# Kernel tuning notes

Hardware: AMD Instinct MI355X
Metric: run time of the kernel (lower is better)

Reference implementation:

```python
import jax, jax.numpy as jnp
import numpy as np

B, L, D, K = 8, 256, 256, 64  # batch, slots, n_input, attn_dimension


def setup_inputs() -> dict:
    key = jax.random.key(0)
    k1, k2, k3 = jax.random.split(key, 3)
    inputs = jax.random.normal(k1, (B, L, D), dtype=jnp.float32)
    # torch.nn.Linear weights are [out_features, in_features]; scale to avoid tanh saturation
    W1 = jax.random.normal(k2, (K, 2 * D), dtype=jnp.float32) * (1.0 / np.sqrt(2 * D))
    W2 = jax.random.normal(k3, (1, K), dtype=jnp.float32) * (1.0 / np.sqrt(K))
    return {"inputs": inputs, "W1": W1, "W2": W2}


def reference(inputs, W1, W2):
    # CONCAT branch of SlotAttention:
    #   score[b,i,j] = W2 @ tanh(W1 @ concat(inputs[b,i], inputs[b,j]))
    # Split W1 into the halves acting on the i-part and j-part of the concat
    # (identical math, avoids materializing the [B,L,L,2D] concat tensor).
    d = inputs.shape[-1]
    W1i, W1j = W1[:, :d], W1[:, d:]
    qi = jnp.einsum('bld,kd->blk', inputs, W1i)          # [B,L,K]
    kj = jnp.einsum('bld,kd->blk', inputs, W1j)          # [B,L,K]
    h = jnp.tanh(qi[:, :, None, :] + kj[:, None, :, :])  # [B,L,L,K]
    scores = jnp.einsum('bijk,k->bij', h, W2[0])         # [B,L,L]
    attn = jax.nn.softmax(scores, axis=2)                # softmax over j
    context = jnp.einsum('bij,bjd->bid', attn, inputs)   # [B,L,D]
    return jnp.concatenate([inputs, context], axis=2)    # [B,L,2D]
```

## Files before the change

### kernel.cpp

```cpp
#include <hip/hip_runtime.h>


#define Bn 8
#define Ln 256
#define Dn 256
#define Kn 64
#define ROWS (Bn*Ln)
#define IPB 4

__global__ __launch_bounds__(128) void proj_kernel(
    const float* __restrict__ X,
    const float* __restrict__ W1,
    float* __restrict__ QK)
{
    __shared__ float Xs[4 * 256];
    const int tid = threadIdx.x;
    const int r0 = blockIdx.x * 4;

    const float4* Xg4 = (const float4*)(X + r0 * Dn);
    float4* Xs4 = (float4*)Xs;
    #pragma unroll
    for (int idx = tid; idx < 256; idx += 128) Xs4[idx] = Xg4[idx];
    __syncthreads();

    const int k = tid & 63, half = tid >> 6;
    const float4* Wrow = (const float4*)(W1 + k * (2 * Dn) + half * Dn);
    float acc[4] = {0, 0, 0, 0};
    #pragma unroll 8
    for (int d4 = 0; d4 < 64; ++d4) {
        float4 w = Wrow[d4];
        #pragma unroll
        for (int r = 0; r < 4; ++r) {
            float4 x = ((const float4*)(Xs + r * Dn))[d4];
            float a = acc[r];
            a = fmaf(w.x, x.x, a);
            a = fmaf(w.y, x.y, a);
            a = fmaf(w.z, x.z, a);
            a = fmaf(w.w, x.w, a);
            acc[r] = a;
        }
    }
    #pragma unroll
    for (int r = 0; r < 4; ++r) {
        float e = __expf(2.0f * acc[r]);
        float t = 1.0f - 2.0f / (e + 1.0f);
        t = fminf(0.99999988f, fmaxf(-0.99999988f, t));
        QK[(r0 + r) * 128 + tid] = t;
    }
}

__global__ __launch_bounds__(256) void attn_kernel(
    const float* __restrict__ X,
    const float* __restrict__ QK,
    const float* __restrict__ W2,
    float* __restrict__ out)
{
    __shared__ float tq_s[IPB * Kn];
    __shared__ float w2_s[Kn];
    __shared__ float S[Ln * IPB];
    __shared__ float4 red[4 * IPB * 64];

    const int tid = threadIdx.x;
    const int b  = blockIdx.x / (Ln / IPB);
    const int i0 = (blockIdx.x % (Ln / IPB)) * IPB;

    if (tid < Kn) w2_s[tid] = W2[tid];
    {
        int ii = tid >> 6, kk = tid & 63;
        tq_s[ii * Kn + kk] = QK[(b * Ln + i0 + ii) * 128 + kk];
    }

    float tkr[Kn];
    const float4* kj4 = (const float4*)(QK + (b * Ln + tid) * 128 + 64);
    #pragma unroll
    for (int q = 0; q < 16; ++q) {
        float4 v = kj4[q];
        tkr[q * 4 + 0] = v.x; tkr[q * 4 + 1] = v.y;
        tkr[q * 4 + 2] = v.z; tkr[q * 4 + 3] = v.w;
    }
    __syncthreads();

    float s[IPB] = {0, 0, 0, 0};
    const float4* w4  = (const float4*)w2_s;
    const float4* q4a = (const float4*)(tq_s);
    const float4* q4b = (const float4*)(tq_s + Kn);
    const float4* q4c = (const float4*)(tq_s + 2 * Kn);
    const float4* q4d = (const float4*)(tq_s + 3 * Kn);
    #pragma unroll
    for (int k4 = 0; k4 < 16; ++k4) {
        float4 w  = w4[k4];
        float4 q0 = q4a[k4], q1 = q4b[k4], q2 = q4c[k4], q3 = q4d[k4];
        #pragma unroll
        for (int c = 0; c < 4; ++c) {
            float tk = tkr[k4 * 4 + c];
            float wk = (c == 0) ? w.x : (c == 1) ? w.y : (c == 2) ? w.z : w.w;
            float tq0 = (c == 0) ? q0.x : (c == 1) ? q0.y : (c == 2) ? q0.z : q0.w;
            float tq1 = (c == 0) ? q1.x : (c == 1) ? q1.y : (c == 2) ? q1.z : q1.w;
            float tq2 = (c == 0) ? q2.x : (c == 1) ? q2.y : (c == 2) ? q2.z : q2.w;
            float tq3 = (c == 0) ? q3.x : (c == 1) ? q3.y : (c == 2) ? q3.z : q3.w;
            float n0 = tq0 + tk, d0 = fmaf(tq0, tk, 1.0f);
            float n1 = tq1 + tk, d1 = fmaf(tq1, tk, 1.0f);
            float n2 = tq2 + tk, d2 = fmaf(tq2, tk, 1.0f);
            float n3 = tq3 + tk, d3 = fmaf(tq3, tk, 1.0f);
            s[0] = fmaf(wk, n0 * __builtin_amdgcn_rcpf(d0), s[0]);
            s[1] = fmaf(wk, n1 * __builtin_amdgcn_rcpf(d1), s[1]);
            s[2] = fmaf(wk, n2 * __builtin_amdgcn_rcpf(d2), s[2]);
            s[3] = fmaf(wk, n3 * __builtin_amdgcn_rcpf(d3), s[3]);
        }
    }
    ((float4*)S)[tid] = make_float4(s[0], s[1], s[2], s[3]);
    __syncthreads();

    {
        const int wv = tid >> 6, lane = tid & 63;
        float v0 = S[(lane      ) * IPB + wv];
        float v1 = S[(lane +  64) * IPB + wv];
        float v2 = S[(lane + 128) * IPB + wv];
        float v3 = S[(lane + 192) * IPB + wv];
        float m = fmaxf(fmaxf(v0, v1), fmaxf(v2, v3));
        #pragma unroll
        for (int off = 32; off > 0; off >>= 1)
            m = fmaxf(m, __shfl_xor(m, off));
        float e0 = __expf(v0 - m), e1 = __expf(v1 - m);
        float e2 = __expf(v2 - m), e3 = __expf(v3 - m);
        float sum = e0 + e1 + e2 + e3;
        #pragma unroll
        for (int off = 32; off > 0; off >>= 1)
            sum += __shfl_xor(sum, off);
        float inv = 1.0f / sum;
        S[(lane      ) * IPB + wv] = e0 * inv;
        S[(lane +  64) * IPB + wv] = e1 * inv;
        S[(lane + 128) * IPB + wv] = e2 * inv;
        S[(lane + 192) * IPB + wv] = e3 * inv;
    }
    __syncthreads();

    {
        const int wv = tid >> 6, lane = tid & 63;
        float4 acc0 = {0,0,0,0}, acc1 = {0,0,0,0}, acc2 = {0,0,0,0}, acc3 = {0,0,0,0};
        const float4* Xb4 = (const float4*)(X + b * Ln * Dn);
        const float4* S4  = (const float4*)S;
        const int jbase = wv * 64;
        #pragma unroll 8
        for (int jj = 0; jj < 64; ++jj) {
            int j = jbase + jj;
            float4 at = S4[j];
            float4 x  = Xb4[j * 64 + lane];
            acc0.x = fmaf(at.x, x.x, acc0.x); acc0.y = fmaf(at.x, x.y, acc0.y);
            acc0.z = fmaf(at.x, x.z, acc0.z); acc0.w = fmaf(at.x, x.w, acc0.w);
            acc1.x = fmaf(at.y, x.x, acc1.x); acc1.y = fmaf(at.y, x.y, acc1.y);
            acc1.z = fmaf(at.y, x.z, acc1.z); acc1.w = fmaf(at.y, x.w, acc1.w);
            acc2.x = fmaf(at.z, x.x, acc2.x); acc2.y = fmaf(at.z, x.y, acc2.y);
            acc2.z = fmaf(at.z, x.z, acc2.z); acc2.w = fmaf(at.z, x.w, acc2.w);
            acc3.x = fmaf(at.w, x.x, acc3.x); acc3.y = fmaf(at.w, x.y, acc3.y);
            acc3.z = fmaf(at.w, x.z, acc3.z); acc3.w = fmaf(at.w, x.w, acc3.w);
        }
        red[(wv * IPB + 0) * 64 + lane] = acc0;
        red[(wv * IPB + 1) * 64 + lane] = acc1;
        red[(wv * IPB + 2) * 64 + lane] = acc2;
        red[(wv * IPB + 3) * 64 + lane] = acc3;
    }
    __syncthreads();

    {
        const int i = tid >> 6, q = tid & 63;
        float4 p0 = red[(0 * IPB + i) * 64 + q];
        float4 p1 = red[(1 * IPB + i) * 64 + q];
        float4 p2 = red[(2 * IPB + i) * 64 + q];
        float4 p3 = red[(3 * IPB + i) * 64 + q];
        float4 c;
        c.x = (p0.x + p1.x) + (p2.x + p3.x);
        c.y = (p0.y + p1.y) + (p2.y + p3.y);
        c.z = (p0.z + p1.z) + (p2.z + p3.z);
        c.w = (p0.w + p1.w) + (p2.w + p3.w);
        const int row = b * Ln + i0 + i;
        float4 xcopy = ((const float4*)(X + row * Dn))[q];
        ((float4*)(out + row * 2 * Dn))[q]      = xcopy;
        ((float4*)(out + row * 2 * Dn + Dn))[q] = c;
    }
}

extern "C" void kernel_launch(void* const* d_in, const int* in_sizes, int n_in,
                              void* d_out, int out_size, void* d_ws, size_t ws_size,
                              hipStream_t stream) {
    const float* X  = (const float*)d_in[0];
    const float* W1 = (const float*)d_in[1];
    const float* W2 = (const float*)d_in[2];
    float* out = (float*)d_out;
    float* QK  = (float*)d_ws;

    proj_kernel<<<ROWS / 4, 128, 0, stream>>>(X, W1, QK);
    attn_kernel<<<ROWS / IPB, 256, 0, stream>>>(X, QK, W2, out);
}
```

Baseline: 83.21 us.

## Rewrite tanh-sum score as per-key partial fraction using precomputed reciprocals

The score term w·tanh(a+b) is rewritten via the tanh addition formula as w·c + w(1−c²)/(tq+c), with c=1/tanh(kj). The projection kernel precomputes c, the coefficient B and the per-key sum of w·c, so the inner loop needs only an add, a reciprocal and an FMA per element instead of two adds, a multiply, a reciprocal and an FMA. Small tanh(kj) values are clamped to 2^-10 to avoid division blow-up. This introduces approximation error and cancellation between large terms when keys are near zero. The projection kernel also moves to 8 rows per 256-thread block.

After: 85.95 us. 1.03x slower.

```diff
diff --git a/kernel.cpp b/kernel.cpp
--- a/kernel.cpp
+++ b/kernel.cpp
@@ -8,30 +8,37 @@
 #define ROWS (Bn*Ln)
 #define IPB 4
 
-__global__ __launch_bounds__(128) void proj_kernel(
+#define TKMIN 9.765625e-4f
+#define TMAX  0.99999988f
+
+__global__ __launch_bounds__(256) void proj_kernel(
     const float* __restrict__ X,
     const float* __restrict__ W1,
-    float* __restrict__ QK)
+    const float* __restrict__ W2,
+    float* __restrict__ TQ,
+    float* __restrict__ CB,
+    float* __restrict__ Cj)
 {
-    __shared__ float Xs[4 * 256];
+    __shared__ float Xs[8 * 256];
     const int tid = threadIdx.x;
-    const int r0 = blockIdx.x * 4;
+    const int r0 = blockIdx.x * 8;
 
     const float4* Xg4 = (const float4*)(X + r0 * Dn);
     float4* Xs4 = (float4*)Xs;
-    #pragma unroll
-    for (int idx = tid; idx < 256; idx += 128) Xs4[idx] = Xg4[idx];
-    __syncthreads();
-
-    const int k = tid & 63, half = tid >> 6;
-    const float4* Wrow = (const float4*)(W1 + k * (2 * Dn) + half * Dn);
+    Xs4[tid]       = Xg4[tid];
+    Xs4[tid + 256] = Xg4[tid + 256];
+    __syncthreads();
+
+    const int kk = tid & 63, half = (tid >> 6) & 1, rg = tid >> 7;
+    const float w2k = W2[kk];
+    const float4* Wrow = (const float4*)(W1 + kk * (2 * Dn) + half * Dn);
     float acc[4] = {0, 0, 0, 0};
     #pragma unroll 8
     for (int d4 = 0; d4 < 64; ++d4) {
         float4 w = Wrow[d4];
         #pragma unroll
         for (int r = 0; r < 4; ++r) {
-            float4 x = ((const float4*)(Xs + r * Dn))[d4];
+            float4 x = ((const float4*)(Xs + (rg * 4 + r) * Dn))[d4];
             float a = acc[r];
             a = fmaf(w.x, x.x, a);
             a = fmaf(w.y, x.y, a);
@@ -42,21 +49,36 @@
     }
     #pragma unroll
     for (int r = 0; r < 4; ++r) {
+        const int row = r0 + rg * 4 + r;
         float e = __expf(2.0f * acc[r]);
         float t = 1.0f - 2.0f / (e + 1.0f);
-        t = fminf(0.99999988f, fmaxf(-0.99999988f, t));
-        QK[(r0 + r) * 128 + tid] = t;
+        t = fminf(TMAX, fmaxf(-TMAX, t));
+        if (half == 0) {
+            TQ[row * Kn + kk] = t;
+        } else {
+            float tk = (fabsf(t) < TKMIN) ? copysignf(TKMIN, t) : t;
+            float c  = __builtin_amdgcn_rcpf(tk);
+            float wc = w2k * c;
+            float Bv = fmaf(-wc, c, w2k);
+            CB[row * 128 + kk]      = c;
+            CB[row * 128 + 64 + kk] = Bv;
+            float vsum = wc;
+            #pragma unroll
+            for (int off = 32; off > 0; off >>= 1)
+                vsum += __shfl_xor(vsum, off);
+            if (kk == 0) Cj[row] = vsum;
+        }
     }
 }
 
-__global__ __launch_bounds__(256) void attn_kernel(
+__global__ __launch_bounds__(256, 2) void attn_kernel(
     const float* __restrict__ X,
-    const float* __restrict__ QK,
-    const float* __restrict__ W2,
+    const float* __restrict__ TQ,
+    const float* __restrict__ CB,
+    const float* __restrict__ Cj,
     float* __restrict__ out)
 {
     __shared__ float tq_s[IPB * Kn];
-    __shared__ float w2_s[Kn];
     __shared__ float S[Ln * IPB];
     __shared__ float4 red[4 * IPB * 64];
 
@@ -64,51 +86,51 @@
     const int b  = blockIdx.x / (Ln / IPB);
     const int i0 = (blockIdx.x % (Ln / IPB)) * IPB;
 
-    if (tid < Kn) w2_s[tid] = W2[tid];
     {
         int ii = tid >> 6, kk = tid & 63;
-        tq_s[ii * Kn + kk] = QK[(b * Ln + i0 + ii) * 128 + kk];
-    }
-
-    float tkr[Kn];
-    const float4* kj4 = (const float4*)(QK + (b * Ln + tid) * 128 + 64);
+        tq_s[ii * Kn + kk] = TQ[(b * Ln + i0 + ii) * Kn + kk];
+    }
+
+    float cr[Kn], Br[Kn];
+    const float4* cb4 = (const float4*)(CB + (b * Ln + tid) * 128);
     #pragma unroll
     for (int q = 0; q < 16; ++q) {
-        float4 v = kj4[q];
-        tkr[q * 4 + 0] = v.x; tkr[q * 4 + 1] = v.y;
-        tkr[q * 4 + 2] = v.z; tkr[q * 4 + 3] = v.w;
-    }
-    __syncthreads();
-
-    float s[IPB] = {0, 0, 0, 0};
-    const float4* w4  = (const float4*)w2_s;
+        float4 v = cb4[q];
+        cr[q * 4 + 0] = v.x; cr[q * 4 + 1] = v.y;
+        cr[q * 4 + 2] = v.z; cr[q * 4 + 3] = v.w;
+    }
+    #pragma unroll
+    for (int q = 0; q < 16; ++q) {
+        float4 v = cb4[16 + q];
+        Br[q * 4 + 0] = v.x; Br[q * 4 + 1] = v.y;
+        Br[q * 4 + 2] = v.z; Br[q * 4 + 3] = v.w;
+    }
+    const float Cjv = Cj[b * Ln + tid];
+    __syncthreads();
+
+    float s0 = Cjv, s1 = Cjv, s2 = Cjv, s3 = Cjv;
     const float4* q4a = (const float4*)(tq_s);
     const float4* q4b = (const float4*)(tq_s + Kn);
     const float4* q4c = (const float4*)(tq_s + 2 * Kn);
     const float4* q4d = (const float4*)(tq_s + 3 * Kn);
     #pragma unroll
     for (int k4 = 0; k4 < 16; ++k4) {
-        float4 w  = w4[k4];
         float4 q0 = q4a[k4], q1 = q4b[k4], q2 = q4c[k4], q3 = q4d[k4];
         #pragma unroll
         for (int c = 0; c < 4; ++c) {
-            float tk = tkr[k4 * 4 + c];
-            float wk = (c == 0) ? w.x : (c == 1) ? w.y : (c == 2) ? w.z : w.w;
+            float ck = cr[k4 * 4 + c];
+            float Bk = Br[k4 * 4 + c];
             float tq0 = (c == 0) ? q0.x : (c == 1) ? q0.y : (c == 2) ? q0.z : q0.w;
             float tq1 = (c == 0) ? q1.x : (c == 1) ? q1.y : (c == 2) ? q1.z : q1.w;
             float tq2 = (c == 0) ? q2.x : (c == 1) ? q2.y : (c == 2) ? q2.z : q2.w;
             float tq3 = (c == 0) ? q3.x : (c == 1) ? q3.y : (c == 2) ? q3.z : q3.w;
-            float n0 = tq0 + tk, d0 = fmaf(tq0, tk, 1.0f);
-            float n1 = tq1 + tk, d1 = fmaf(tq1, tk, 1.0f);
-            float n2 = tq2 + tk, d2 = fmaf(tq2, tk, 1.0f);
-            float n3 = tq3 + tk, d3 = fmaf(tq3, tk, 1.0f);
-            s[0] = fmaf(wk, n0 * __builtin_amdgcn_rcpf(d0), s[0]);
-            s[1] = fmaf(wk, n1 * __builtin_amdgcn_rcpf(d1), s[1]);
-            s[2] = fmaf(wk, n2 * __builtin_amdgcn_rcpf(d2), s[2]);
-            s[3] = fmaf(wk, n3 * __builtin_amdgcn_rcpf(d3), s[3]);
-        }
-    }
-    ((float4*)S)[tid] = make_float4(s[0], s[1], s[2], s[3]);
+            s0 = fmaf(Bk, __builtin_amdgcn_rcpf(tq0 + ck), s0);
+            s1 = fmaf(Bk, __builtin_amdgcn_rcpf(tq1 + ck), s1);
+            s2 = fmaf(Bk, __builtin_amdgcn_rcpf(tq2 + ck), s2);
+            s3 = fmaf(Bk, __builtin_amdgcn_rcpf(tq3 + ck), s3);
+        }
+    }
+    ((float4*)S)[tid] = make_float4(s0, s1, s2, s3);
     __syncthreads();
 
     {
@@ -187,8 +209,11 @@
     const float* W1 = (const float*)d_in[1];
     const float* W2 = (const float*)d_in[2];
     float* out = (float*)d_out;
-    float* QK  = (float*)d_ws;
-
-    proj_kernel<<<ROWS / 4, 128, 0, stream>>>(X, W1, QK);
-    attn_kernel<<<ROWS / IPB, 256, 0, stream>>>(X, QK, W2, out);
+
+    float* TQ = (float*)d_ws;
+    float* CB = (float*)((char*)d_ws + (512 << 10));
+    float* Cj = (float*)((char*)d_ws + (1536 << 10));
+
+    proj_kernel<<<ROWS / 8, 256, 0, stream>>>(X, W1, W2, TQ, CB, Cj);
+    attn_kernel<<<ROWS / IPB, 256, 0, stream>>>(X, TQ, CB, Cj, out);
 }
```

## Process eight query rows per attention block to raise reuse of keys and X

Applied to the files above, without the earlier changes.

Doubles the number of query rows handled by each attention block from four to eight. Each thread's register copy of the key projection and each load of X are now reused across twice as many rows, and the launch uses half as many blocks. The scores are split into two shared arrays so the softmax and context passes keep their four-wide layout. The cost is more registers per thread and more shared memory for the reduction buffer, which may lower occupancy, and fewer blocks to spread across the GPU.

Measured after the change: 84.93 us. 2.1% more time.

```diff
diff --git a/kernel.cpp b/kernel.cpp
--- a/kernel.cpp
+++ b/kernel.cpp
@@ -6,7 +6,7 @@
 #define Dn 256
 #define Kn 64
 #define ROWS (Bn*Ln)
-#define IPB 4
+#define IPB 8
 
 __global__ __launch_bounds__(128) void proj_kernel(
     const float* __restrict__ X,
@@ -57,17 +57,20 @@
 {
     __shared__ float tq_s[IPB * Kn];
     __shared__ float w2_s[Kn];
-    __shared__ float S[Ln * IPB];
+    __shared__ float S0[Ln * 4];
+    __shared__ float S1[Ln * 4];
     __shared__ float4 red[4 * IPB * 64];
 
     const int tid = threadIdx.x;
-    const int b  = blockIdx.x / (Ln / IPB);
-    const int i0 = (blockIdx.x % (Ln / IPB)) * IPB;
+    const int b  = blockIdx.x >> 5;
+    const int i0 = (blockIdx.x & 31) * IPB;
 
     if (tid < Kn) w2_s[tid] = W2[tid];
-    {
-        int ii = tid >> 6, kk = tid & 63;
-        tq_s[ii * Kn + kk] = QK[(b * Ln + i0 + ii) * 128 + kk];
+    #pragma unroll
+    for (int e = 0; e < 2; ++e) {
+        int idx = e * 256 + tid;
+        int ii = idx >> 6, kk = idx & 63;
+        tq_s[idx] = QK[(b * Ln + i0 + ii) * 128 + kk];
     }
 
     float tkr[Kn];
@@ -80,90 +83,114 @@
     }
     __syncthreads();
 
-    float s[IPB] = {0, 0, 0, 0};
-    const float4* w4  = (const float4*)w2_s;
-    const float4* q4a = (const float4*)(tq_s);
-    const float4* q4b = (const float4*)(tq_s + Kn);
-    const float4* q4c = (const float4*)(tq_s + 2 * Kn);
-    const float4* q4d = (const float4*)(tq_s + 3 * Kn);
+    float s[IPB] = {0, 0, 0, 0, 0, 0, 0, 0};
+    const float4* w4 = (const float4*)w2_s;
     #pragma unroll
     for (int k4 = 0; k4 < 16; ++k4) {
-        float4 w  = w4[k4];
-        float4 q0 = q4a[k4], q1 = q4b[k4], q2 = q4c[k4], q3 = q4d[k4];
+        float4 w = w4[k4];
+        float4 q[IPB];
+        #pragma unroll
+        for (int i = 0; i < IPB; ++i)
+            q[i] = ((const float4*)(tq_s + i * Kn))[k4];
         #pragma unroll
         for (int c = 0; c < 4; ++c) {
             float tk = tkr[k4 * 4 + c];
             float wk = (c == 0) ? w.x : (c == 1) ? w.y : (c == 2) ? w.z : w.w;
-            float tq0 = (c == 0) ? q0.x : (c == 1) ? q0.y : (c == 2) ? q0.z : q0.w;
-            float tq1 = (c == 0) ? q1.x : (c == 1) ? q1.y : (c == 2) ? q1.z : q1.w;
-            float tq2 = (c == 0) ? q2.x : (c == 1) ? q2.y : (c == 2) ? q2.z : q2.w;
-            float tq3 = (c == 0) ? q3.x : (c == 1) ? q3.y : (c == 2) ? q3.z : q3.w;
-            float n0 = tq0 + tk, d0 = fmaf(tq0, tk, 1.0f);
-            float n1 = tq1 + tk, d1 = fmaf(tq1, tk, 1.0f);
-            float n2 = tq2 + tk, d2 = fmaf(tq2, tk, 1.0f);
-            float n3 = tq3 + tk, d3 = fmaf(tq3, tk, 1.0f);
-            s[0] = fmaf(wk, n0 * __builtin_amdgcn_rcpf(d0), s[0]);
-            s[1] = fmaf(wk, n1 * __builtin_amdgcn_rcpf(d1), s[1]);
-            s[2] = fmaf(wk, n2 * __builtin_amdgcn_rcpf(d2), s[2]);
-            s[3] = fmaf(wk, n3 * __builtin_amdgcn_rcpf(d3), s[3]);
-        }
-    }
-    ((float4*)S)[tid] = make_float4(s[0], s[1], s[2], s[3]);
+            #pragma unroll
+            for (int i = 0; i < IPB; ++i) {
+                float tq = (c == 0) ? q[i].x : (c == 1) ? q[i].y
+                         : (c == 2) ? q[i].z : q[i].w;
+                float n = tq + tk, d = fmaf(tq, tk, 1.0f);
+                s[i] = fmaf(wk, n * __builtin_amdgcn_rcpf(d), s[i]);
+            }
+        }
+    }
+    ((float4*)S0)[tid] = make_float4(s[0], s[1], s[2], s[3]);
+    ((float4*)S1)[tid] = make_float4(s[4], s[5], s[6], s[7]);
     __syncthreads();
 
     {
         const int wv = tid >> 6, lane = tid & 63;
-        float v0 = S[(lane      ) * IPB + wv];
-        float v1 = S[(lane +  64) * IPB + wv];
-        float v2 = S[(lane + 128) * IPB + wv];
-        float v3 = S[(lane + 192) * IPB + wv];
-        float m = fmaxf(fmaxf(v0, v1), fmaxf(v2, v3));
-        #pragma unroll
-        for (int off = 32; off > 0; off >>= 1)
-            m = fmaxf(m, __shfl_xor(m, off));
-        float e0 = __expf(v0 - m), e1 = __expf(v1 - m);
-        float e2 = __expf(v2 - m), e3 = __expf(v3 - m);
-        float sum = e0 + e1 + e2 + e3;
-        #pragma unroll
-        for (int off = 32; off > 0; off >>= 1)
-            sum += __shfl_xor(sum, off);
-        float inv = 1.0f / sum;
-        S[(lane      ) * IPB + wv] = e0 * inv;
-        S[(lane +  64) * IPB + wv] = e1 * inv;
-        S[(lane + 128) * IPB + wv] = e2 * inv;
-        S[(lane + 192) * IPB + wv] = e3 * inv;
+        float v0 = S0[(lane      ) * 4 + wv];
+        float v1 = S0[(lane +  64) * 4 + wv];
+        float v2 = S0[(lane + 128) * 4 + wv];
+        float v3 = S0[(lane + 192) * 4 + wv];
+        float u0 = S1[(lane      ) * 4 + wv];
+        float u1 = S1[(lane +  64) * 4 + wv];
+        float u2 = S1[(lane + 128) * 4 + wv];
+        float u3 = S1[(lane + 192) * 4 + wv];
+        float mv = fmaxf(fmaxf(v0, v1), fmaxf(v2, v3));
+        float mu = fmaxf(fmaxf(u0, u1), fmaxf(u2, u3));
+        #pragma unroll
+        for (int off = 32; off > 0; off >>= 1) {
+            mv = fmaxf(mv, __shfl_xor(mv, off));
+            mu = fmaxf(mu, __shfl_xor(mu, off));
+        }
+        float e0 = __expf(v0 - mv), e1 = __expf(v1 - mv);
+        float e2 = __expf(v2 - mv), e3 = __expf(v3 - mv);
+        float f0 = __expf(u0 - mu), f1 = __expf(u1 - mu);
+        float f2 = __expf(u2 - mu), f3 = __expf(u3 - mu);
+        float sv = e0 + e1 + e2 + e3;
+        float su = f0 + f1 + f2 + f3;
+        #pragma unroll
+        for (int off = 32; off > 0; off >>= 1) {
+            sv += __shfl_xor(sv, off);
+            su += __shfl_xor(su, off);
+        }
+        float iv = 1.0f / sv, iu = 1.0f / su;
+        S0[(lane      ) * 4 + wv] = e0 * iv;
+        S0[(lane +  64) * 4 + wv] = e1 * iv;
+        S0[(lane + 128) * 4 + wv] = e2 * iv;
+        S0[(lane + 192) * 4 + wv] = e3 * iv;
+        S1[(lane      ) * 4 + wv] = f0 * iu;
+        S1[(lane +  64) * 4 + wv] = f1 * iu;
+        S1[(lane + 128) * 4 + wv] = f2 * iu;
+        S1[(lane + 192) * 4 + wv] = f3 * iu;
     }
     __syncthreads();
 
     {
         const int wv = tid >> 6, lane = tid & 63;
-        float4 acc0 = {0,0,0,0}, acc1 = {0,0,0,0}, acc2 = {0,0,0,0}, acc3 = {0,0,0,0};
+        float4 a[IPB];
+        #pragma unroll
+        for (int i = 0; i < IPB; ++i) a[i] = make_float4(0.f, 0.f, 0.f, 0.f);
         const float4* Xb4 = (const float4*)(X + b * Ln * Dn);
-        const float4* S4  = (const float4*)S;
+        const float4* S04 = (const float4*)S0;
+        const float4* S14 = (const float4*)S1;
         const int jbase = wv * 64;
-        #pragma unroll 8
+        #pragma unroll 4
         for (int jj = 0; jj < 64; ++jj) {
             int j = jbase + jj;
-            float4 at = S4[j];
-            float4 x  = Xb4[j * 64 + lane];
-            acc0.x = fmaf(at.x, x.x, acc0.x); acc0.y = fmaf(at.x, x.y, acc0.y);
-            acc0.z = fmaf(at.x, x.z, acc0.z); acc0.w = fmaf(at.x, x.w, acc0.w);
-            acc1.x = fmaf(at.y, x.x, acc1.x); acc1.y = fmaf(at.y, x.y, acc1.y);
-            acc1.z = fmaf(at.y, x.z, acc1.z); acc1.w = fmaf(at.y, x.w, acc1.w);
-            acc2.x = fmaf(at.z, x.x, acc2.x); acc2.y = fmaf(at.z, x.y, acc2.y);
-            acc2.z = fmaf(at.z, x.z, acc2.z); acc2.w = fmaf(at.z, x.w, acc2.w);
-            acc3.x = fmaf(at.w, x.x, acc3.x); acc3.y = fmaf(at.w, x.y, acc3.y);
-            acc3.z = fmaf(at.w, x.z, acc3.z); acc3.w = fmaf(at.w, x.w, acc3.w);
-        }
-        red[(wv * IPB + 0) * 64 + lane] = acc0;
-        red[(wv * IPB + 1) * 64 + lane] = acc1;
-        red[(wv * IPB + 2) * 64 + lane] = acc2;
-        red[(wv * IPB + 3) * 64 + lane] = acc3;
-    }
-    __syncthreads();
-
-    {
-        const int i = tid >> 6, q = tid & 63;
+            float4 at0 = S04[j];
+            float4 at1 = S14[j];
+            float4 x   = Xb4[j * 64 + lane];
+            a[0].x = fmaf(at0.x, x.x, a[0].x); a[0].y = fmaf(at0.x, x.y, a[0].y);
+            a[0].z = fmaf(at0.x, x.z, a[0].z); a[0].w = fmaf(at0.x, x.w, a[0].w);
+            a[1].x = fmaf(at0.y, x.x, a[1].x); a[1].y = fmaf(at0.y, x.y, a[1].y);
+            a[1].z = fmaf(at0.y, x.z, a[1].z); a[1].w = fmaf(at0.y, x.w, a[1].w);
+            a[2].x = fmaf(at0.z, x.x, a[2].x); a[2].y = fmaf(at0.z, x.y, a[2].y);
+            a[2].z = fmaf(at0.z, x.z, a[2].z); a[2].w = fmaf(at0.z, x.w, a[2].w);
+            a[3].x = fmaf(at0.w, x.x, a[3].x); a[3].y = fmaf(at0.w, x.y, a[3].y);
+            a[3].z = fmaf(at0.w, x.z, a[3].z); a[3].w = fmaf(at0.w, x.w, a[3].w);
+            a[4].x = fmaf(at1.x, x.x, a[4].x); a[4].y = fmaf(at1.x, x.y, a[4].y);
+            a[4].z = fmaf(at1.x, x.z, a[4].z); a[4].w = fmaf(at1.x, x.w, a[4].w);
+            a[5].x = fmaf(at1.y, x.x, a[5].x); a[5].y = fmaf(at1.y, x.y, a[5].y);
+            a[5].z = fmaf(at1.y, x.z, a[5].z); a[5].w = fmaf(at1.y, x.w, a[5].w);
+            a[6].x = fmaf(at1.z, x.x, a[6].x); a[6].y = fmaf(at1.z, x.y, a[6].y);
+            a[6].z = fmaf(at1.z, x.z, a[6].z); a[6].w = fmaf(at1.z, x.w, a[6].w);
+            a[7].x = fmaf(at1.w, x.x, a[7].x); a[7].y = fmaf(at1.w, x.y, a[7].y);
+            a[7].z = fmaf(at1.w, x.z, a[7].z); a[7].w = fmaf(at1.w, x.w, a[7].w);
+        }
+        #pragma unroll
+        for (int i = 0; i < IPB; ++i)
+            red[(wv * IPB + i) * 64 + lane] = a[i];
+    }
+    __syncthreads();
+
+    #pragma unroll
+    for (int e = 0; e < 2; ++e) {
+        const int idx = e * 256 + tid;
+        const int i = idx >> 6, q = idx & 63;
         float4 p0 = red[(0 * IPB + i) * 64 + q];
         float4 p1 = red[(1 * IPB + i) * 64 + q];
         float4 p2 = red[(2 * IPB + i) * 64 + q];
```
